# Optimization experiments

Measured on AMD Instinct MI355X. Metric: run time of the kernel, lower is better.

The kernel has to match this reference:

```python
import jax, jax.numpy as jnp
import numpy as np
import math
from jax import lax

D = 256      # d_model = out_channel
NH = 8       # n_heads
DEP = D // NH
DFF = 1024
B = 48       # conv batch == attended axis in this model
CIN = 32
HW = 32
S = 30 * 30  # (HW-2)**2 after 3x3 valid conv
OUT = 1
FMAX = float(np.finfo(np.float32).max)


def _p(k, shp, scale=0.02):
    return jax.random.normal(k, shp, jnp.float32) * scale


def setup_inputs():
    key = jax.random.key(0)
    ks = jax.random.split(key, 34)
    return {
        'X_en': jax.random.normal(ks[0], (B, CIN, HW, HW), jnp.float32),
        'X_de': jax.random.normal(ks[1], (B, CIN, HW, HW), jnp.float32),
        'conv1_w': _p(ks[2], (D, CIN, 3, 3)), 'conv1_b': _p(ks[3], (D,)),
        'conv2_w': _p(ks[4], (D, D, 3, 3)), 'conv2_b': _p(ks[5], (D,)),
        'enc_wq': _p(ks[6], (D, D)), 'enc_wk': _p(ks[7], (D, D)), 'enc_wv': _p(ks[8], (D, D)),
        'enc_rel_w': _p(ks[9], (S, NH, DEP, B)),
        'enc_ffn_w1': _p(ks[10], (DFF, D)), 'enc_ffn_b1': _p(ks[11], (DFF,)),
        'enc_ffn_w2': _p(ks[12], (D, DFF)), 'enc_ffn_b2': _p(ks[13], (D,)),
        'dec_m_wq': _p(ks[14], (D, D)), 'dec_m_wk': _p(ks[15], (D, D)), 'dec_m_wv': _p(ks[16], (D, D)),
        'dec_m_rel_w': _p(ks[17], (S, NH, DEP, B)),
        'dec_m_lin1_w': _p(ks[18], (B, B)), 'dec_m_lin1_b': _p(ks[19], (B,)),
        'dec_m_lin2_w': _p(ks[20], (B, B)), 'dec_m_lin2_b': _p(ks[21], (B,)),
        'dec_c_wq': _p(ks[22], (D, D)), 'dec_c_wk': _p(ks[23], (D, D)), 'dec_c_wv': _p(ks[24], (D, D)),
        'dec_c_rel_w': _p(ks[25], (S, NH, DEP, B)),
        'dec_ffn_w1': _p(ks[26], (DFF, D)), 'dec_ffn_b1': _p(ks[27], (DFF,)),
        'dec_ffn_w2': _p(ks[28], (D, DFF)), 'dec_ffn_b2': _p(ks[29], (D,)),
        'out_w': _p(ks[30], (OUT, D)), 'out_b': _p(ks[31], (OUT,)),
    }


def _ln(x, eps=1e-5):
    m = jnp.mean(x, -1, keepdims=True)
    v = jnp.mean((x - m) ** 2, -1, keepdims=True)
    return (x - m) / jnp.sqrt(v + eps)


def _skew(q, w):
    # Music-Transformer relative-position skew: matmul + pad + reshape + slice
    emd = jnp.einsum('shbd,shdj->shbj', q, w)  # (S,NH,b,b)
    s, h, i, j = emd.shape
    l = i + j - 1
    x = jnp.concatenate([emd, jnp.zeros_like(emd)], -1).reshape(s, h, -1)
    pad = (-x.shape[-1]) % l
    x = jnp.pad(x, ((0, 0), (0, 0), (0, pad)))
    return x.reshape(s, h, -1, l)[:, :, :i, i - 1:]


def _mha(xq, xk, xv, wq, wk, wv, rel_w, lins=None):
    b, sl, d = xq.shape
    # raw view (not transpose): (b,sl,d) -> (sl,b,NH,DEP), then swap to (sl,NH,b,DEP)
    q = (xq @ wq.T).reshape(sl, b, NH, DEP).swapaxes(1, 2)
    k = (xk @ wk.T).reshape(sl, b, NH, DEP).swapaxes(1, 2)
    v = (xv @ wv.T).reshape(sl, b, NH, DEP).swapaxes(1, 2)
    scores = jnp.einsum('shid,shjd->shij', q, k) / math.sqrt(DEP)  # (sl,NH,b,b)
    if lins is not None:  # masked path: per-call linears + causal mask
        l1w, l1b, l2w, l2b = lins
        qk = scores @ l1w.T + l1b
        qk = jnp.swapaxes(qk, 2, 3) @ l2w.T + l2b
        mask = jnp.triu(jnp.full((b, b), -FMAX, jnp.float32), 1)
        bmm = qk + mask
    else:
        bmm = scores  # linear1/linear2 outputs are discarded when mask=False
    attn = jax.nn.softmax(bmm + _skew(q, rel_w), axis=0)  # softmax over dim 0 (S)
    out = jnp.einsum('shij,shjd->shid', attn, v)  # (sl,NH,b,DEP)
    return out.reshape(b, sl, NH * DEP)  # view(a_s[2], a_s[0], -1)


def reference(X_en, X_de, conv1_w, conv1_b, conv2_w, conv2_b, enc_wq, enc_wk, enc_wv, enc_rel_w, enc_ffn_w1, enc_ffn_b1, enc_ffn_w2, enc_ffn_b2, dec_m_wq, dec_m_wk, dec_m_wv, dec_m_rel_w, dec_m_lin1_w, dec_m_lin1_b, dec_m_lin2_w, dec_m_lin2_b, dec_c_wq, dec_c_wk, dec_c_wv, dec_c_rel_w, dec_ffn_w1, dec_ffn_b1, dec_ffn_w2, dec_ffn_b2, out_w, out_b):
    def conv(x, w, b_, pad):
        y = lax.conv_general_dilated(x, w, (1, 1), [(pad, pad), (pad, pad)],
                                     dimension_numbers=('NCHW', 'OIHW', 'NCHW'))
        return y + b_[None, :, None, None]

    def convs(x):
        return conv(conv(x, conv1_w, conv1_b, 0), conv2_w, conv2_b, 1)

    xpe = convs(X_en)
    xpd = convs(X_de)
    b, d, h, w = xpe.shape
    x_en = xpe.reshape(b, h * w, d)  # raw reshape as in torch source
    x_de = xpd.reshape(b, h * w, d)
    # encoder layer
    a = _mha(x_en, x_en, x_en, enc_wq, enc_wk, enc_wv, enc_rel_w)
    o1 = _ln(x_en + a)
    f = jax.nn.relu(o1 @ enc_ffn_w1.T + enc_ffn_b1) @ enc_ffn_w2.T + enc_ffn_b2
    enc_out = _ln(o1 + f)
    # decoder layer
    m = _mha(x_de, x_de, x_de, dec_m_wq, dec_m_wk, dec_m_wv, dec_m_rel_w,
             (dec_m_lin1_w, dec_m_lin1_b, dec_m_lin2_w, dec_m_lin2_b))
    h1 = _ln(x_de + m)
    c = _mha(h1, enc_out, enc_out, dec_c_wq, dec_c_wk, dec_c_wv, dec_c_rel_w)
    h2 = _ln(c + h1)
    f2 = jax.nn.relu(h2 @ dec_ffn_w1.T + dec_ffn_b1) @ dec_ffn_w2.T + dec_ffn_b2
    h3 = _ln(h2 + f2)
    y = h3 @ out_w.T + out_b
    return jax.nn.softmax(y, axis=0)
```

## Files before the change

### kernel.cpp

```cpp
#include <hip/hip_runtime.h>
#include <float.h>

typedef __bf16 bf16;
typedef __attribute__((ext_vector_type(8))) __bf16 bf16x8;
typedef __attribute__((ext_vector_type(4))) __bf16 bf16x4;
typedef __attribute__((ext_vector_type(4))) float f32x4;

__device__ __forceinline__ int imin(int a, int b) { return a < b ? a : b; }

__device__ __forceinline__ void gl2lds(const bf16* g, bf16* l) {
  __builtin_amdgcn_global_load_lds(
      (const __attribute__((address_space(1))) void*)g,
      (__attribute__((address_space(3))) void*)l, 16, 0, 0);
}

__global__ void k_prep_misc(bf16* zp, const float* __restrict__ l1w,
                            const float* __restrict__ l2w,
                            bf16* __restrict__ L1p, bf16* __restrict__ L2p) {
  zp[threadIdx.x] = (bf16)0.0f;
  for (int i = threadIdx.x; i < 3456; i += 256) {
    int r = i / 72, c = i - r * 72;
    L1p[i] = (c < 48) ? (bf16)l1w[r * 48 + c] : (bf16)0.0f;
    L2p[i] = (c < 48) ? (bf16)l2w[r * 48 + c] : (bf16)0.0f;
  }
}

struct CastSegs { const float* s[13]; bf16* d[13]; int n[13]; };
__global__ void k_cast_all(CastSegs sg, int total) {
  int i = blockIdx.x * 256 + threadIdx.x;
  if (i >= total) return;
  for (int k = 0; k < 13; ++k) {
    if (i < sg.n[k]) { sg.d[k][i] = (bf16)sg.s[k][i]; return; }
    i -= sg.n[k];
  }
}

__global__ __launch_bounds__(256) void k_prep_rel(const float* __restrict__ rel,
                                                  bf16* __restrict__ RelT) {
  __shared__ float tile[32 * 49];
  const int t = threadIdx.x;
  for (int u = 0; u < 8; ++u) {
    const size_t sh = (size_t)blockIdx.x * 8 + u;
    const float* src = rel + sh * 1536;
    bf16* dst = RelT + sh * 1536;
    __syncthreads();
    for (int i = t; i < 1536; i += 256) {
      int k = i / 48, j = i - k * 48;
      tile[k * 49 + j] = src[i];
    }
    __syncthreads();
    for (int i = t; i < 1536; i += 256) {
      int j = i >> 5, k = i & 31;
      dst[i] = (bf16)tile[k * 49 + j];
    }
  }
}

__global__ void k_prep_x(const float* __restrict__ XE, const float* __restrict__ XD,
                         bf16* __restrict__ XR) {
  int idx = blockIdx.x * 256 + threadIdx.x;
  if (idx >= 96 * 1024 * 32) return;
  int b = idx >> 15, r = idx & 32767, pos = r >> 5, ic = r & 31;
  const float* X = (b < 48) ? XE : XD;
  int bl = (b < 48) ? b : b - 48;
  XR[idx] = (bf16)X[((size_t)(bl * 32 + ic) << 10) + pos];
}

__global__ void k_pack_conv(const float* __restrict__ w, bf16* __restrict__ dst,
                            int OC, int IC, int total) {
  int idx = blockIdx.x * 256 + threadIdx.x;
  if (idx >= total) return;
  int t = idx / (OC * IC);
  int rem = idx - t * OC * IC;
  int oc = rem / IC, ic = rem - oc * IC;
  dst[idx] = (bf16)w[(size_t)(oc * IC + ic) * 9 + t];
}

__global__ __launch_bounds__(256, 2) void k_gemm128(
    const bf16* __restrict__ A, const bf16* __restrict__ A2,
    const bf16* __restrict__ B, const bf16* __restrict__ B2, int nsplit,
    const float* __restrict__ bias, bf16* __restrict__ C,
    int M, int N, int K, int relu, int ldc, int coff) {
  __shared__ alignas(16) bf16 SM[32768];
  const int t = threadIdx.x, wave = t >> 6;
  const int lane = t & 63, fr = lane & 15, kq = lane >> 4;
  const int wm = wave & 1, wn = wave >> 1;
  const int m0 = blockIdx.x * 128, n0 = blockIdx.y * 128;
  const bf16* Ause = A; const bf16* Buse = B; int nloc = n0;
  if (n0 >= nsplit) { Ause = A2; Buse = B2; nloc = n0 - nsplit; }
  const int srow = t >> 3;
  const int sg8 = (((t & 7) ^ (srow & 7)) << 3);
  const bf16* gA[4]; const bf16* gB[4];
#pragma unroll
  for (int r = 0; r < 4; ++r) {
    gA[r] = Ause + (size_t)imin(m0 + r * 32 + srow, M - 1) * K + sg8;
    gB[r] = Buse + (size_t)(nloc + r * 32 + srow) * K + sg8;
  }
  const int swz = (kq ^ (fr & 7)) << 3;
  const int aoff = (wm * 64 + fr) * 64 + swz;
  const int boff = 8192 + (wn * 64 + fr) * 64 + swz;
  f32x4 acc[4][4] = {};
  const int NU = K >> 6;
  {
    bf16* db = SM + wave * 512;
#pragma unroll
    for (int r = 0; r < 4; ++r) gl2lds(gA[r], db + r * 2048);
#pragma unroll
    for (int r = 0; r < 4; ++r) gl2lds(gB[r], db + 8192 + r * 2048);
  }
  __syncthreads();
  for (int u = 0; u < NU; ++u) {
    const int cur = u & 1;
    if (u + 1 < NU) {
      bf16* db = SM + (cur ^ 1) * 16384 + wave * 512;
      const int kb = (u + 1) << 6;
#pragma unroll
      for (int r = 0; r < 4; ++r) gl2lds(gA[r] + kb, db + r * 2048);
#pragma unroll
      for (int r = 0; r < 4; ++r) gl2lds(gB[r] + kb, db + 8192 + r * 2048);
    }
    const bf16* buf = SM + cur * 16384;
    bf16x8 af[2][4], bw[2][4];
#pragma unroll
    for (int kk = 0; kk < 2; ++kk) {
      const int xo = kk << 5;
#pragma unroll
      for (int mt = 0; mt < 4; ++mt)
        af[kk][mt] = *(const bf16x8*)(buf + ((aoff + mt * 1024) ^ xo));
#pragma unroll
      for (int nt = 0; nt < 4; ++nt)
        bw[kk][nt] = *(const bf16x8*)(buf + ((boff + nt * 1024) ^ xo));
    }
#pragma unroll
    for (int kk = 0; kk < 2; ++kk)
#pragma unroll
      for (int mt = 0; mt < 4; ++mt)
#pragma unroll
        for (int nt = 0; nt < 4; ++nt)
          acc[mt][nt] = __builtin_amdgcn_mfma_f32_16x16x32_bf16(af[kk][mt], bw[kk][nt], acc[mt][nt], 0, 0, 0);
    __syncthreads();
  }
  bf16* Cst = SM;
  for (int half = 0; half < 2; ++half) {
    if (wm == half) {
      for (int mt = 0; mt < 4; ++mt)
        for (int nt = 0; nt < 4; ++nt) {
          int n = n0 + wn * 64 + nt * 16 + fr;
          float bv = bias ? bias[n] : 0.0f;
          for (int r = 0; r < 4; ++r) {
            float v = acc[mt][nt][r] + bv;
            if (relu) v = fmaxf(v, 0.0f);
            Cst[(mt * 16 + kq * 4 + r) * 128 + wn * 64 + nt * 16 + fr] = (bf16)v;
          }
        }
    }
    __syncthreads();
    for (int i = t; i < 1024; i += 256) {
      int r = i >> 4, cs = i & 15;
      int gm = m0 + half * 64 + r;
      if (gm < M)
        *(bf16x8*)(C + (size_t)gm * ldc + coff + n0 + cs * 8) = *(const bf16x8*)(Cst + r * 128 + cs * 8);
    }
    __syncthreads();
  }
}

template <int CIN, int PAD, int SRCW, int SRCROWS, int CHECK, int TRANS, int MTOT>
__global__ __launch_bounds__(256, 2) void k_conv128(
    const bf16* __restrict__ A, const bf16* __restrict__ Bp,
    const float* __restrict__ bias, bf16* __restrict__ C,
    const bf16* __restrict__ zpage) {
  __shared__ alignas(16) bf16 SM[8192];
  bf16* As = SM;
  bf16* Bs = SM + 4096;
  const int t = threadIdx.x, wave = t >> 6;
  const int lane = t & 63, fr = lane & 15, kq = lane >> 4;
  const int wm = wave & 1, wn = wave >> 1;
  const int m0 = blockIdx.x * 128, n0 = blockIdx.y * 128;
  const int srow = t >> 2, kseg = (t & 3) * 8;
  f32x4 acc[4][4] = {};
  int bb[2], yy[2], xx[2];
  for (int hf = 0; hf < 2; ++hf) {
    int m = imin(m0 + hf * 64 + srow, MTOT - 1);
    int b = m / 900, p = m - b * 900;
    bb[hf] = b; yy[hf] = p / 30; xx[hf] = p - (p / 30) * 30;
  }
  bf16* sA0 = As + wave * 512;
  bf16* sA1 = As + 2048 + wave * 512;
  bf16* sB0 = Bs + wave * 512;
  bf16* sB1 = Bs + 2048 + wave * 512;
  for (int k0 = 0; k0 < CIN; k0 += 32) {
    for (int t9 = 0; t9 < 9; ++t9) {
      const int ky = t9 / 3, kx = t9 - ky * 3;
      const bf16* ga[2];
      for (int hf = 0; hf < 2; ++hf) {
        int sy = yy[hf] + ky - PAD, sx = xx[hf] + kx - PAD;
        bool valid = !CHECK || (sy >= 0 && sy < SRCW && sx >= 0 && sx < SRCW);
        ga[hf] = (valid ? A + (size_t)(bb[hf] * SRCROWS + sy * SRCW + sx) * CIN : zpage) + kseg;
      }
      const bf16* gb = Bp + (size_t)(t9 * 256 + n0 + srow) * CIN + kseg;
      gl2lds(ga[0] + k0, sA0);
      gl2lds(ga[1] + k0, sA1);
      gl2lds(gb + k0, sB0);
      gl2lds(gb + (size_t)64 * CIN + k0, sB1);
      __syncthreads();
      bf16x8 af[4], bw[4];
      for (int mt = 0; mt < 4; ++mt)
        af[mt] = *(const bf16x8*)(As + (wm * 64 + mt * 16 + fr) * 32 + kq * 8);
      for (int nt = 0; nt < 4; ++nt)
        bw[nt] = *(const bf16x8*)(Bs + (wn * 64 + nt * 16 + fr) * 32 + kq * 8);
      for (int mt = 0; mt < 4; ++mt)
        for (int nt = 0; nt < 4; ++nt)
          acc[mt][nt] = __builtin_amdgcn_mfma_f32_16x16x32_bf16(af[mt], bw[nt], acc[mt][nt], 0, 0, 0);
      __syncthreads();
    }
  }
  bf16* Cst = SM;
  for (int half = 0; half < 2; ++half) {
    if (wm == half) {
      for (int mt = 0; mt < 4; ++mt)
        for (int nt = 0; nt < 4; ++nt) {
          int n = n0 + wn * 64 + nt * 16 + fr;
          float bv = bias[n];
          for (int r = 0; r < 4; ++r) {
            float v = acc[mt][nt][r] + bv;
            if (TRANS)
              Cst[(wn * 64 + nt * 16 + fr) * 64 + mt * 16 + kq * 4 + r] = (bf16)v;
            else
              Cst[(mt * 16 + kq * 4 + r) * 128 + wn * 64 + nt * 16 + fr] = (bf16)v;
          }
        }
    }
    __syncthreads();
    if (TRANS) {
      for (int i = t; i < 2048; i += 256) {
        int oc = i >> 4, pc = i & 15;
        int gm = m0 + half * 64 + pc * 4;
        if (gm < MTOT) {
          int b = gm / 900, p = gm - b * 900;
          *(bf16x4*)(C + (size_t)(b * 256 + n0 + oc) * 900 + p) = *(const bf16x4*)(Cst + oc * 64 + pc * 4);
        }
      }
    } else {
      for (int i = t; i < 1024; i += 256) {
        int r = i >> 4, cs = i & 15;
        int gm = m0 + half * 64 + r;
        if (gm < MTOT)
          *(bf16x8*)(C + (size_t)gm * 256 + n0 + cs * 8) = *(const bf16x8*)(Cst + r * 128 + cs * 8);
      }
    }
    __syncthreads();
  }
}

__global__ __launch_bounds__(256, 2) void k_conv2x(
    const bf16* __restrict__ A, const bf16* __restrict__ Bp,
    const float* __restrict__ bias, bf16* __restrict__ C,
    const bf16* __restrict__ zpage) {
  __shared__ alignas(16) bf16 SM[32768];
  const int t = threadIdx.x, wave = t >> 6;
  const int lane = t & 63, fr = lane & 15, kq = lane >> 4;
  const int wm = wave & 1, wn = wave >> 1;
  const int m0 = blockIdx.x * 128, n0 = blockIdx.y * 128;
  const int srow = t >> 3;
  const int sg8 = (((t & 7) ^ (srow & 7)) << 3);
  int pb[4], py[4], px[4];
#pragma unroll
  for (int r = 0; r < 4; ++r) {
    int m = imin(m0 + r * 32 + srow, 86399);
    int b = m / 900, p = m - b * 900;
    pb[r] = b * 900; py[r] = p / 30; px[r] = p - (p / 30) * 30;
  }
  const int swz = (kq ^ (fr & 7)) << 3;
  const int aoff = (wm * 64 + fr) * 64 + swz;
  const int boff = 8192 + (wn * 64 + fr) * 64 + swz;
  f32x4 acc[4][4] = {};
  auto stage = [&](int u, int bsel) {
    const int t9 = u >> 2, k0c = (u & 3) << 6;
    const int ky = t9 / 3, kx = t9 - ky * 3;
    bf16* db = SM + bsel * 16384 + wave * 512;
#pragma unroll
    for (int r = 0; r < 4; ++r) {
      int sy = py[r] + ky - 1, sx = px[r] + kx - 1;
      bool valid = (sy >= 0 && sy < 30 && sx >= 0 && sx < 30);
      const bf16* g = valid ? (A + (size_t)(pb[r] + sy * 30 + sx) * 256 + k0c + sg8)
                            : (zpage + sg8);
      gl2lds(g, db + r * 2048);
    }
    const bf16* gb = Bp + (size_t)(t9 * 256 + n0 + srow) * 256 + k0c + sg8;
#pragma unroll
    for (int r = 0; r < 4; ++r)
      gl2lds(gb + (size_t)r * 32 * 256, db + 8192 + r * 2048);
  };
  stage(0, 0);
  __syncthreads();
  for (int u = 0; u < 36; ++u) {
    const int cur = u & 1;
    if (u < 35) stage(u + 1, cur ^ 1);
    const bf16* buf = SM + cur * 16384;
    bf16x8 af[2][4], bw[2][4];
#pragma unroll
    for (int kk = 0; kk < 2; ++kk) {
      const int xo = kk << 5;
#pragma unroll
      for (int mt = 0; mt < 4; ++mt)
        af[kk][mt] = *(const bf16x8*)(buf + ((aoff + mt * 1024) ^ xo));
#pragma unroll
      for (int nt = 0; nt < 4; ++nt)
        bw[kk][nt] = *(const bf16x8*)(buf + ((boff + nt * 1024) ^ xo));
    }
#pragma unroll
    for (int kk = 0; kk < 2; ++kk)
#pragma unroll
      for (int mt = 0; mt < 4; ++mt)
#pragma unroll
        for (int nt = 0; nt < 4; ++nt)
          acc[mt][nt] = __builtin_amdgcn_mfma_f32_16x16x32_bf16(af[kk][mt], bw[kk][nt], acc[mt][nt], 0, 0, 0);
    __syncthreads();
  }
  bf16* Cst = SM;
  for (int half = 0; half < 2; ++half) {
    if (wm == half) {
      for (int mt = 0; mt < 4; ++mt)
        for (int nt = 0; nt < 4; ++nt) {
          int n = n0 + wn * 64 + nt * 16 + fr;
          float bv = bias[n];
          for (int r = 0; r < 4; ++r) {
            float v = acc[mt][nt][r] + bv;
            Cst[(wn * 64 + nt * 16 + fr) * 64 + mt * 16 + kq * 4 + r] = (bf16)v;
          }
        }
    }
    __syncthreads();
    for (int i = t; i < 2048; i += 256) {
      int oc = i >> 4, pc = i & 15;
      int gm = m0 + half * 64 + pc * 4;
      int b = gm / 900, p = gm - b * 900;
      *(bf16x4*)(C + (size_t)(b * 256 + n0 + oc) * 900 + p) = *(const bf16x4*)(Cst + oc * 64 + pc * 4);
    }
    __syncthreads();
  }
}

template <int MASKED>
__global__ __launch_bounds__(256, MASKED ? 4 : 5) void k_attn_z(
    const bf16* __restrict__ QKV, const bf16* __restrict__ RelT, bf16* __restrict__ Z,
    const bf16* __restrict__ L1p, const bf16* __restrict__ L2p,
    const float* __restrict__ l1b, const float* __restrict__ l2b) {
  __shared__ alignas(16) bf16 QKs[2][48 * 40];
  __shared__ float EMD[48 * 49];
  __shared__ alignas(16) bf16 zst[48 * 48];
  __shared__ alignas(16) bf16 Sc[MASKED ? 48 * 72 : 8];
  __shared__ alignas(16) bf16 T2b[MASKED ? 48 * 72 : 8];
  const int sh = blockIdx.x, s = sh >> 3, h = sh & 7;
  const int t = threadIdx.x, wave = t >> 6, lane = t & 63, fr = lane & 15, kq = lane >> 4;
  const float scale = 0.17677669529663687f;
  for (int c = t; c < 384; c += 256) {
    int half = c >= 192 ? 1 : 0, cc = c - half * 192;
    int row = cc >> 2, seg = cc & 3;
    *(bf16x8*)(&QKs[half][row * 40 + seg * 8]) =
        *(const bf16x8*)(QKV + (size_t)(s * 48 + row) * 768 + half * 256 + h * 32 + seg * 8);
  }
  if constexpr (MASKED) {
    for (int i = t; i < 768; i += 256) {
      int r = i >> 4, c = 48 + (i & 15);
      Sc[r * 72 + c] = (bf16)0.0f;
      T2b[r * 72 + c] = (bf16)0.0f;
    }
  }
  __syncthreads();
  const bf16* relb = RelT + (size_t)sh * 1536;
  f32x4 sreg[3];
  int u = 0;
  for (int t9 = wave; t9 < 9; t9 += 4, ++u) {
    int ti = t9 / 3, tj = t9 - ti * 3;
    bf16x8 af = *(const bf16x8*)(&QKs[0][(ti * 16 + fr) * 40 + kq * 8]);
    bf16x8 bk = *(const bf16x8*)(&QKs[1][(tj * 16 + fr) * 40 + kq * 8]);
    bf16x8 rf = *(const bf16x8*)(relb + (tj * 16 + fr) * 32 + kq * 8);
    f32x4 sacc = {}, eacc = {};
    sacc = __builtin_amdgcn_mfma_f32_16x16x32_bf16(af, bk, sacc, 0, 0, 0);
    eacc = __builtin_amdgcn_mfma_f32_16x16x32_bf16(af, rf, eacc, 0, 0, 0);
    for (int r = 0; r < 4; ++r)
      EMD[(ti * 16 + kq * 4 + r) * 49 + tj * 16 + fr] = eacc[r];
    if constexpr (MASKED) {
      for (int r = 0; r < 4; ++r)
        Sc[(ti * 16 + kq * 4 + r) * 72 + tj * 16 + fr] = (bf16)(sacc[r] * scale);
    } else {
      for (int r = 0; r < 4; ++r) sreg[u][r] = sacc[r] * scale;
    }
  }
  __syncthreads();
  if constexpr (!MASKED) {
    u = 0;
    for (int t9 = wave; t9 < 9; t9 += 4, ++u) {
      int ti = t9 / 3, tj = t9 - ti * 3;
      for (int r = 0; r < 4; ++r) {
        int i = ti * 16 + kq * 4 + r, j = tj * 16 + fr;
        float v = sreg[u][r];
        if (j <= i) v += EMD[i * 49 + 47 + j - i];
        zst[i * 48 + j] = (bf16)v;
      }
    }
  } else {
    for (int t9 = wave; t9 < 9; t9 += 4) {
      int ti = t9 / 3, tj = t9 - ti * 3;
      f32x4 a2 = {};
      for (int k0 = 0; k0 < 64; k0 += 32) {
        bf16x8 af = *(const bf16x8*)(Sc + (ti * 16 + fr) * 72 + k0 + kq * 8);
        bf16x8 bw = *(const bf16x8*)(L1p + (tj * 16 + fr) * 72 + k0 + kq * 8);
        a2 = __builtin_amdgcn_mfma_f32_16x16x32_bf16(af, bw, a2, 0, 0, 0);
      }
      for (int r = 0; r < 4; ++r) {
        int i = ti * 16 + kq * 4 + r, a = tj * 16 + fr;
        T2b[a * 72 + i] = (bf16)(a2[r] + l1b[a]);
      }
    }
    __syncthreads();
    for (int t9 = wave; t9 < 9; t9 += 4) {
      int ti = t9 / 3, tj = t9 - ti * 3;
      f32x4 a2 = {};
      for (int k0 = 0; k0 < 64; k0 += 32) {
        bf16x8 af = *(const bf16x8*)(T2b + (ti * 16 + fr) * 72 + k0 + kq * 8);
        bf16x8 bw = *(const bf16x8*)(L2p + (tj * 16 + fr) * 72 + k0 + kq * 8);
        a2 = __builtin_amdgcn_mfma_f32_16x16x32_bf16(af, bw, a2, 0, 0, 0);
      }
      for (int r = 0; r < 4; ++r) {
        int aa = ti * 16 + kq * 4 + r, cc = tj * 16 + fr;
        float v;
        if (cc > aa) v = -10000.0f;
        else v = a2[r] + l2b[cc] + EMD[aa * 49 + 47 + cc - aa];
        zst[aa * 48 + cc] = (bf16)v;
      }
    }
  }
  __syncthreads();
  bf16* zb = Z + (size_t)sh * 2304;
  for (int c = t; c < 288; c += 256)
    *(bf16x8*)(zb + c * 8) = *(const bf16x8*)(zst + c * 8);
}

__global__ __launch_bounds__(256) void k_colstats(const bf16* __restrict__ Z,
                                                  float* __restrict__ Mc, float* __restrict__ Ic) {
  __shared__ float rm[32][72], rs[32][72];
  const int t = threadIdx.x, cg = t & 7, sg = t >> 3;
  const bf16* p = Z + blockIdx.x * 64 + cg * 8;
  const int s0 = sg * 29, s1 = imin(900, s0 + 29);
  float m[8], ss[8];
  for (int e = 0; e < 8; ++e) { m[e] = -FLT_MAX; ss[e] = 0.0f; }
  for (int s = s0; s < s1; ++s) {
    bf16x8 zv = *(const bf16x8*)(p + (size_t)s * 18432);
    for (int e = 0; e < 8; ++e) {
      float v = (float)zv[e];
      if (v > m[e]) { ss[e] *= __expf(m[e] - v); m[e] = v; }
      ss[e] += __expf(v - m[e]);
    }
  }
  for (int e = 0; e < 8; ++e) { rm[sg][cg * 8 + e] = m[e]; rs[sg][cg * 8 + e] = ss[e]; }
  __syncthreads();
  if (t < 64) {
    float M2 = -FLT_MAX;
    for (int g = 0; g < 32; ++g) M2 = fmaxf(M2, rm[g][t]);
    float S2 = 0.0f;
    for (int g = 0; g < 32; ++g) S2 += rs[g][t] * __expf(rm[g][t] - M2);
    Mc[blockIdx.x * 64 + t] = M2;
    Ic[blockIdx.x * 64 + t] = 1.0f / S2;
  }
}

__global__ __launch_bounds__(256, 6) void k_attn_av(
    const bf16* __restrict__ Z, const bf16* __restrict__ QKV,
    const float* __restrict__ Mc, const float* __restrict__ Ic, bf16* __restrict__ O) {
  __shared__ alignas(16) bf16 Ps[48 * 72];
  __shared__ alignas(16) bf16 Vt[32 * 72];
  __shared__ alignas(16) bf16 Ost[48 * 32];
  const int sh = blockIdx.x, s = sh >> 3, h = sh & 7;
  const int t = threadIdx.x, wave = t >> 6, lane = t & 63, fr = lane & 15, kq = lane >> 4;
  for (int i = t; i < 768; i += 256) Ps[(i >> 4) * 72 + 48 + (i & 15)] = (bf16)0.0f;
  for (int i = t; i < 512; i += 256) Vt[(i >> 4) * 72 + 48 + (i & 15)] = (bf16)0.0f;
  const bf16* zb = Z + (size_t)sh * 2304;
  const float* mc = Mc + h * 2304;
  const float* ic = Ic + h * 2304;
  for (int c = t; c < 288; c += 256) {
    int r = c / 6, seg = c - r * 6;
    int idx = r * 48 + seg * 8;
    bf16x8 zv = *(const bf16x8*)(zb + idx);
    f32x4 m0v = *(const f32x4*)(mc + idx), m1v = *(const f32x4*)(mc + idx + 4);
    f32x4 i0v = *(const f32x4*)(ic + idx), i1v = *(const f32x4*)(ic + idx + 4);
    bf16x8 pv;
    for (int e = 0; e < 4; ++e) pv[e] = (bf16)(__expf((float)zv[e] - m0v[e]) * i0v[e]);
    for (int e = 0; e < 4; ++e) pv[4 + e] = (bf16)(__expf((float)zv[4 + e] - m1v[e]) * i1v[e]);
    *(bf16x8*)(Ps + r * 72 + seg * 8) = pv;
  }
  for (int c = t; c < 192; c += 256) {
    int j = c >> 2, seg = c & 3;
    bf16x8 v = *(const bf16x8*)(QKV + (size_t)(s * 48 + j) * 768 + 512 + h * 32 + seg * 8);
    for (int e = 0; e < 8; ++e) Vt[(seg * 8 + e) * 72 + j] = v[e];
  }
  __syncthreads();
  for (int t6 = wave; t6 < 6; t6 += 4) {
    int ti = t6 >> 1, td = t6 & 1;
    f32x4 a2 = {};
    for (int k0 = 0; k0 < 64; k0 += 32) {
      bf16x8 af = *(const bf16x8*)(Ps + (ti * 16 + fr) * 72 + k0 + kq * 8);
      bf16x8 bv = *(const bf16x8*)(Vt + (td * 16 + fr) * 72 + k0 + kq * 8);
      a2 = __builtin_amdgcn_mfma_f32_16x16x32_bf16(af, bv, a2, 0, 0, 0);
    }
    for (int r = 0; r < 4; ++r)
      Ost[(ti * 16 + kq * 4 + r) * 32 + td * 16 + fr] = (bf16)a2[r];
  }
  __syncthreads();
  bf16* ob = O + (size_t)sh * 1536;
  for (int c = t; c < 192; c += 256)
    *(bf16x8*)(ob + c * 8) = *(const bf16x8*)(Ost + c * 8);
}

__global__ __launch_bounds__(256) void k_add_ln(
    const bf16* __restrict__ Xa, const bf16* __restrict__ Xb, bf16* __restrict__ out) {
  const int t = threadIdx.x, lane = t & 63, w = t >> 6;
  const size_t off = ((size_t)blockIdx.x * 4 + w) * 256 + lane * 4;
  bf16x4 av = *(const bf16x4*)(Xa + off);
  bf16x4 bv = *(const bf16x4*)(Xb + off);
  f32x4 x;
  for (int c = 0; c < 4; ++c) x[c] = (float)av[c] + (float)bv[c];
  float sum = x[0] + x[1] + x[2] + x[3];
  for (int o = 1; o < 64; o <<= 1) sum += __shfl_xor(sum, o);
  float mean = sum * (1.0f / 256.0f);
  float q = 0.0f;
  for (int c = 0; c < 4; ++c) { float d = x[c] - mean; q += d * d; }
  for (int o = 1; o < 64; o <<= 1) q += __shfl_xor(q, o);
  float rstd = rsqrtf(q * (1.0f / 256.0f) + 1e-5f);
  bf16x4 y;
  for (int c = 0; c < 4; ++c) y[c] = (bf16)((x[c] - mean) * rstd);
  *(bf16x4*)(out + off) = y;
}

__global__ __launch_bounds__(256) void k_ydot(
    const bf16* __restrict__ H, const float* __restrict__ w,
    const float* __restrict__ b, float* __restrict__ Y) {
  const int t = threadIdx.x, lane = t & 63, wv = t >> 6;
  const size_t row = (size_t)blockIdx.x * 4 + wv;
  bf16x4 hx = *(const bf16x4*)(H + row * 256 + lane * 4);
  f32x4 ww = *(const f32x4*)(w + lane * 4);
  float s = (float)hx[0] * ww[0] + (float)hx[1] * ww[1] + (float)hx[2] * ww[2] + (float)hx[3] * ww[3];
  for (int o = 1; o < 64; o <<= 1) s += __shfl_xor(s, o);
  if (lane == 0) Y[row] = s + b[0];
}

__global__ void k_softmax48(const float* __restrict__ Y, float* __restrict__ O) {
  int ss = blockIdx.x * 256 + threadIdx.x;
  if (ss >= 900) return;
  float m = -FLT_MAX;
  for (int b = 0; b < 48; ++b) m = fmaxf(m, Y[b * 900 + ss]);
  float sum = 0.0f;
  for (int b = 0; b < 48; ++b) sum += __expf(Y[b * 900 + ss] - m);
  float inv = 1.0f / sum;
  for (int b = 0; b < 48; ++b) O[b * 900 + ss] = __expf(Y[b * 900 + ss] - m) * inv;
}

extern "C" void kernel_launch(void* const* d_in, const int* in_sizes, int n_in,
                              void* d_out, int out_size, void* d_ws, size_t ws_size,
                              hipStream_t stream) {
  (void)in_sizes; (void)n_in; (void)out_size;
  const float* X_en = (const float*)d_in[0];
  const float* X_de = (const float*)d_in[1];
  const float* conv1_w = (const float*)d_in[2];
  const float* conv1_b = (const float*)d_in[3];
  const float* conv2_w = (const float*)d_in[4];
  const float* conv2_b = (const float*)d_in[5];
  const float* enc_wq = (const float*)d_in[6];
  const float* enc_wk = (const float*)d_in[7];
  const float* enc_wv = (const float*)d_in[8];
  const float* enc_rel = (const float*)d_in[9];
  const float* enc_f1w = (const float*)d_in[10];
  const float* enc_f1b = (const float*)d_in[11];
  const float* enc_f2w = (const float*)d_in[12];
  const float* enc_f2b = (const float*)d_in[13];
  const float* dm_wq = (const float*)d_in[14];
  const float* dm_wk = (const float*)d_in[15];
  const float* dm_wv = (const float*)d_in[16];
  const float* dm_rel = (const float*)d_in[17];
  const float* dm_l1w = (const float*)d_in[18];
  const float* dm_l1b = (const float*)d_in[19];
  const float* dm_l2w = (const float*)d_in[20];
  const float* dm_l2b = (const float*)d_in[21];
  const float* dc_wq = (const float*)d_in[22];
  const float* dc_wk = (const float*)d_in[23];
  const float* dc_wv = (const float*)d_in[24];
  const float* dc_rel = (const float*)d_in[25];
  const float* d_f1w = (const float*)d_in[26];
  const float* d_f1b = (const float*)d_in[27];
  const float* d_f2w = (const float*)d_in[28];
  const float* d_f2b = (const float*)d_in[29];
  const float* out_w = (const float*)d_in[30];
  const float* out_b = (const float*)d_in[31];
  float* OUT = (float*)d_out;

  const size_t SLOT = 22118400;
  char* ws = (char*)d_ws;
  size_t o = 0;
  bf16* S1 = (bf16*)(ws + o); o += SLOT;
  bf16* S2 = (bf16*)(ws + o); o += SLOT;
  bf16* S3 = (bf16*)(ws + o); o += SLOT;
  bf16* S4 = (bf16*)(ws + o); o += SLOT;
  bf16* S5 = (bf16*)(ws + o); o += SLOT;
  char* U = ws + o; o += 33177600 + 3 * SLOT;
  bf16* Zb = (bf16*)U;
  bf16* QKV = (bf16*)(U + 33177600);
  bf16* XR = (bf16*)U;
  bf16* C1R = (bf16*)(U + 12582912);
  bf16* HID = (bf16*)U;
  bf16* wa = (bf16*)(ws + o); o += 4603904 + 16384;
  float* Y = (float*)(ws + o); o += 172800;
  if (ws_size < o) return;

  bf16* zpage = (bf16*)Y;
  float* encM = (float*)S4; float* encI = encM + 18432;
  float* dmM  = (float*)S3; float* dmI  = dmM + 18432;
  float* crM  = (float*)S2; float* crI  = crM + 18432;
  bf16* encRel = S3;
  bf16* dmRel  = S5;
  bf16* crRel  = S3;

  bf16* c1p = wa;
  bf16* c2p = wa + 73728;
  bf16* EQKVw = wa + 663552;
  bf16* MQKVw = wa + 860160;
  bf16* cqw = wa + 1056768;
  bf16* CKVw = wa + 1122304;
  bf16* ef1 = wa + 1253376;
  bf16* ef2 = wa + 1515520;
  bf16* df1 = wa + 1777664;
  bf16* df2 = wa + 2039808;
  bf16* L1p = wa + 2301952;
  bf16* L2p = wa + 2305408;

  auto gemm = [&](const bf16* A, const bf16* B, const float* bias, bf16* C,
                  int M, int N, int K, int relu, int ldc, int coff) {
    k_gemm128<<<dim3((M + 127) / 128, N / 128), dim3(256), 0, stream>>>(
        A, A, B, B, N, bias, C, M, N, K, relu, ldc, coff);
  };

  k_prep_misc<<<dim3(1), dim3(256), 0, stream>>>(zpage, dm_l1w, dm_l2w, L1p, L2p);
  k_pack_conv<<<dim3(288), dim3(256), 0, stream>>>(conv1_w, c1p, 256, 32, 73728);
  k_pack_conv<<<dim3(2304), dim3(256), 0, stream>>>(conv2_w, c2p, 256, 256, 589824);
  {
    CastSegs sg;
    const float* srcs[13] = {enc_wq, enc_wk, enc_wv, dm_wq, dm_wk, dm_wv, dc_wq,
                             dc_wk, dc_wv, enc_f1w, enc_f2w, d_f1w, d_f2w};
    bf16* dsts[13] = {EQKVw, EQKVw + 65536, EQKVw + 131072, MQKVw, MQKVw + 65536,
                      MQKVw + 131072, cqw, CKVw, CKVw + 65536, ef1, ef2, df1, df2};
    int ns[13] = {65536, 65536, 65536, 65536, 65536, 65536, 65536, 65536, 65536,
                  262144, 262144, 262144, 262144};
    int total = 0;
    for (int k = 0; k < 13; ++k) { sg.s[k] = srcs[k]; sg.d[k] = dsts[k]; sg.n[k] = ns[k]; total += ns[k]; }
    k_cast_all<<<dim3((total + 255) / 256), dim3(256), 0, stream>>>(sg, total);
  }

  k_prep_x<<<dim3(12288), dim3(256), 0, stream>>>(X_en, X_de, XR);
  k_conv128<32, 0, 32, 1024, 0, 0, 86400><<<dim3(675, 2), dim3(256), 0, stream>>>(
      XR, c1p, conv1_b, C1R, zpage);
  k_conv2x<<<dim3(675, 2), dim3(256), 0, stream>>>(C1R, c2p, conv2_b, S1, zpage);

  gemm(S1, EQKVw, nullptr, QKV, 43200, 768, 256, 0, 768, 0);
  k_prep_rel<<<dim3(900), dim3(256), 0, stream>>>(enc_rel, encRel);
  k_attn_z<0><<<dim3(7200), dim3(256), 0, stream>>>(QKV, encRel, Zb, nullptr, nullptr, nullptr, nullptr);
  k_colstats<<<dim3(288), dim3(256), 0, stream>>>(Zb, encM, encI);
  k_attn_av<<<dim3(7200), dim3(256), 0, stream>>>(Zb, QKV, encM, encI, S5);
  k_add_ln<<<dim3(10800), dim3(256), 0, stream>>>(S1, S5, S3);
  gemm(S3, ef1, enc_f1b, HID, 43200, 1024, 256, 1, 1024, 0);
  gemm(HID, ef2, enc_f2b, S5, 43200, 256, 1024, 0, 256, 0);
  k_add_ln<<<dim3(10800), dim3(256), 0, stream>>>(S3, S5, S1);

  gemm(S2, MQKVw, nullptr, QKV, 43200, 768, 256, 0, 768, 0);
  k_prep_rel<<<dim3(900), dim3(256), 0, stream>>>(dm_rel, dmRel);
  k_attn_z<1><<<dim3(7200), dim3(256), 0, stream>>>(QKV, dmRel, Zb, L1p, L2p, dm_l1b, dm_l2b);
  k_colstats<<<dim3(288), dim3(256), 0, stream>>>(Zb, dmM, dmI);
  k_attn_av<<<dim3(7200), dim3(256), 0, stream>>>(Zb, QKV, dmM, dmI, S5);
  k_add_ln<<<dim3(10800), dim3(256), 0, stream>>>(S2, S5, S4);

  k_gemm128<<<dim3(338, 6), dim3(256), 0, stream>>>(
      S4, S1, cqw, CKVw, 256, nullptr, QKV, 43200, 768, 256, 0, 768, 0);
  k_prep_rel<<<dim3(900), dim3(256), 0, stream>>>(dc_rel, crRel);
  k_attn_z<0><<<dim3(7200), dim3(256), 0, stream>>>(QKV, crRel, Zb, nullptr, nullptr, nullptr, nullptr);
  k_colstats<<<dim3(288), dim3(256), 0, stream>>>(Zb, crM, crI);
  k_attn_av<<<dim3(7200), dim3(256), 0, stream>>>(Zb, QKV, crM, crI, S5);
  k_add_ln<<<dim3(10800), dim3(256), 0, stream>>>(S5, S4, S3);

  gemm(S3, df1, d_f1b, HID, 43200, 1024, 256, 1, 1024, 0);
  gemm(HID, df2, d_f2b, S5, 43200, 256, 1024, 0, 256, 0);
  k_add_ln<<<dim3(10800), dim3(256), 0, stream>>>(S3, S5, S4);
  k_ydot<<<dim3(10800), dim3(256), 0, stream>>>(S4, out_w, out_b, Y);
  k_softmax48<<<dim3(4), dim3(256), 0, stream>>>(Y, OUT);
}
```

Baseline: 1.106 ms.

## Single-buffer LDS in GEMM and conv2 kernels, pad epilogue staging

Drops double-buffered LDS prefetching in k_gemm128 and k_conv2x in favour of a single 32KB buffer with load-sync-compute-sync per K step. It also reorders the conv K loop so channel blocks are outermost, and pads the epilogue staging rows (136/68) to reduce LDS bank conflicts. Halving LDS and shrinking fragment register arrays aims at higher occupancy, but global-load latency is no longer overlapped with MFMA work inside a block. The staging buffer still fits, since 64 rows x 136 = 8704 and 128 x 68 = 8704 elements are under 16384.

```diff
diff --git a/kernel.cpp b/kernel.cpp
--- a/kernel.cpp
+++ b/kernel.cpp
@@ -81,7 +81,7 @@
     const bf16* __restrict__ B, const bf16* __restrict__ B2, int nsplit,
     const float* __restrict__ bias, bf16* __restrict__ C,
     int M, int N, int K, int relu, int ldc, int coff) {
-  __shared__ alignas(16) bf16 SM[32768];
+  __shared__ alignas(16) bf16 SM[16384];
   const int t = threadIdx.x, wave = t >> 6;
   const int lane = t & 63, fr = lane & 15, kq = lane >> 4;
   const int wm = wave & 1, wn = wave >> 1;
@@ -100,44 +100,29 @@
   const int aoff = (wm * 64 + fr) * 64 + swz;
   const int boff = 8192 + (wn * 64 + fr) * 64 + swz;
   f32x4 acc[4][4] = {};
-  const int NU = K >> 6;
-  {
+  for (int k0 = 0; k0 < K; k0 += 64) {
     bf16* db = SM + wave * 512;
 #pragma unroll
-    for (int r = 0; r < 4; ++r) gl2lds(gA[r], db + r * 2048);
-#pragma unroll
-    for (int r = 0; r < 4; ++r) gl2lds(gB[r], db + 8192 + r * 2048);
-  }
-  __syncthreads();
-  for (int u = 0; u < NU; ++u) {
-    const int cur = u & 1;
-    if (u + 1 < NU) {
-      bf16* db = SM + (cur ^ 1) * 16384 + wave * 512;
-      const int kb = (u + 1) << 6;
-#pragma unroll
-      for (int r = 0; r < 4; ++r) gl2lds(gA[r] + kb, db + r * 2048);
-#pragma unroll
-      for (int r = 0; r < 4; ++r) gl2lds(gB[r] + kb, db + 8192 + r * 2048);
-    }
-    const bf16* buf = SM + cur * 16384;
-    bf16x8 af[2][4], bw[2][4];
+    for (int r = 0; r < 4; ++r) gl2lds(gA[r] + k0, db + r * 2048);
+#pragma unroll
+    for (int r = 0; r < 4; ++r) gl2lds(gB[r] + k0, db + 8192 + r * 2048);
+    __syncthreads();
 #pragma unroll
     for (int kk = 0; kk < 2; ++kk) {
       const int xo = kk << 5;
+      bf16x8 af[4], bw[4];
 #pragma unroll
       for (int mt = 0; mt < 4; ++mt)
-        af[kk][mt] = *(const bf16x8*)(buf + ((aoff + mt * 1024) ^ xo));
+        af[mt] = *(const bf16x8*)(SM + ((aoff + mt * 1024) ^ xo));
 #pragma unroll
       for (int nt = 0; nt < 4; ++nt)
-        bw[kk][nt] = *(const bf16x8*)(buf + ((boff + nt * 1024) ^ xo));
-    }
-#pragma unroll
-    for (int kk = 0; kk < 2; ++kk)
+        bw[nt] = *(const bf16x8*)(SM + ((boff + nt * 1024) ^ xo));
 #pragma unroll
       for (int mt = 0; mt < 4; ++mt)
 #pragma unroll
         for (int nt = 0; nt < 4; ++nt)
-          acc[mt][nt] = __builtin_amdgcn_mfma_f32_16x16x32_bf16(af[kk][mt], bw[kk][nt], acc[mt][nt], 0, 0, 0);
+          acc[mt][nt] = __builtin_amdgcn_mfma_f32_16x16x32_bf16(af[mt], bw[nt], acc[mt][nt], 0, 0, 0);
+    }
     __syncthreads();
   }
   bf16* Cst = SM;
@@ -150,7 +135,7 @@
           for (int r = 0; r < 4; ++r) {
             float v = acc[mt][nt][r] + bv;
             if (relu) v = fmaxf(v, 0.0f);
-            Cst[(mt * 16 + kq * 4 + r) * 128 + wn * 64 + nt * 16 + fr] = (bf16)v;
+            Cst[(mt * 16 + kq * 4 + r) * 136 + wn * 64 + nt * 16 + fr] = (bf16)v;
           }
         }
     }
@@ -159,7 +144,7 @@
       int r = i >> 4, cs = i & 15;
       int gm = m0 + half * 64 + r;
       if (gm < M)
-        *(bf16x8*)(C + (size_t)gm * ldc + coff + n0 + cs * 8) = *(const bf16x8*)(Cst + r * 128 + cs * 8);
+        *(bf16x8*)(C + (size_t)gm * ldc + coff + n0 + cs * 8) = *(const bf16x8*)(Cst + r * 136 + cs * 8);
     }
     __syncthreads();
   }
@@ -257,7 +242,7 @@
     const bf16* __restrict__ A, const bf16* __restrict__ Bp,
     const float* __restrict__ bias, bf16* __restrict__ C,
     const bf16* __restrict__ zpage) {
-  __shared__ alignas(16) bf16 SM[32768];
+  __shared__ alignas(16) bf16 SM[16384];
   const int t = threadIdx.x, wave = t >> 6;
   const int lane = t & 63, fr = lane & 15, kq = lane >> 4;
   const int wm = wave & 1, wn = wave >> 1;
@@ -275,48 +260,41 @@
   const int aoff = (wm * 64 + fr) * 64 + swz;
   const int boff = 8192 + (wn * 64 + fr) * 64 + swz;
   f32x4 acc[4][4] = {};
-  auto stage = [&](int u, int bsel) {
-    const int t9 = u >> 2, k0c = (u & 3) << 6;
-    const int ky = t9 / 3, kx = t9 - ky * 3;
-    bf16* db = SM + bsel * 16384 + wave * 512;
-#pragma unroll
-    for (int r = 0; r < 4; ++r) {
-      int sy = py[r] + ky - 1, sx = px[r] + kx - 1;
-      bool valid = (sy >= 0 && sy < 30 && sx >= 0 && sx < 30);
-      const bf16* g = valid ? (A + (size_t)(pb[r] + sy * 30 + sx) * 256 + k0c + sg8)
-                            : (zpage + sg8);
-      gl2lds(g, db + r * 2048);
-    }
-    const bf16* gb = Bp + (size_t)(t9 * 256 + n0 + srow) * 256 + k0c + sg8;
-#pragma unroll
-    for (int r = 0; r < 4; ++r)
-      gl2lds(gb + (size_t)r * 32 * 256, db + 8192 + r * 2048);
-  };
-  stage(0, 0);
-  __syncthreads();
-  for (int u = 0; u < 36; ++u) {
-    const int cur = u & 1;
-    if (u < 35) stage(u + 1, cur ^ 1);
-    const bf16* buf = SM + cur * 16384;
-    bf16x8 af[2][4], bw[2][4];
-#pragma unroll
-    for (int kk = 0; kk < 2; ++kk) {
-      const int xo = kk << 5;
-#pragma unroll
-      for (int mt = 0; mt < 4; ++mt)
-        af[kk][mt] = *(const bf16x8*)(buf + ((aoff + mt * 1024) ^ xo));
-#pragma unroll
-      for (int nt = 0; nt < 4; ++nt)
-        bw[kk][nt] = *(const bf16x8*)(buf + ((boff + nt * 1024) ^ xo));
-    }
-#pragma unroll
-    for (int kk = 0; kk < 2; ++kk)
-#pragma unroll
-      for (int mt = 0; mt < 4; ++mt)
+  for (int k0 = 0; k0 < 256; k0 += 64) {
+    for (int t9 = 0; t9 < 9; ++t9) {
+      const int ky = t9 / 3, kx = t9 - ky * 3;
+      bf16* db = SM + wave * 512;
+#pragma unroll
+      for (int r = 0; r < 4; ++r) {
+        int sy = py[r] + ky - 1, sx = px[r] + kx - 1;
+        bool valid = (sy >= 0 && sy < 30 && sx >= 0 && sx < 30);
+        const bf16* g = valid ? (A + (size_t)(pb[r] + sy * 30 + sx) * 256 + k0 + sg8)
+                              : (zpage + sg8);
+        gl2lds(g, db + r * 2048);
+      }
+#pragma unroll
+      for (int r = 0; r < 4; ++r)
+        gl2lds(Bp + (size_t)(t9 * 256 + n0 + r * 32 + srow) * 256 + k0 + sg8,
+               db + 8192 + r * 2048);
+      __syncthreads();
+#pragma unroll
+      for (int kk = 0; kk < 2; ++kk) {
+        const int xo = kk << 5;
+        bf16x8 af[4], bw[4];
+#pragma unroll
+        for (int mt = 0; mt < 4; ++mt)
+          af[mt] = *(const bf16x8*)(SM + ((aoff + mt * 1024) ^ xo));
 #pragma unroll
         for (int nt = 0; nt < 4; ++nt)
-          acc[mt][nt] = __builtin_amdgcn_mfma_f32_16x16x32_bf16(af[kk][mt], bw[kk][nt], acc[mt][nt], 0, 0, 0);
-    __syncthreads();
+          bw[nt] = *(const bf16x8*)(SM + ((boff + nt * 1024) ^ xo));
+#pragma unroll
+        for (int mt = 0; mt < 4; ++mt)
+#pragma unroll
+          for (int nt = 0; nt < 4; ++nt)
+            acc[mt][nt] = __builtin_amdgcn_mfma_f32_16x16x32_bf16(af[mt], bw[nt], acc[mt][nt], 0, 0, 0);
+      }
+      __syncthreads();
+    }
   }
   bf16* Cst = SM;
   for (int half = 0; half < 2; ++half) {
@@ -327,7 +305,7 @@
           float bv = bias[n];
           for (int r = 0; r < 4; ++r) {
             float v = acc[mt][nt][r] + bv;
-            Cst[(wn * 64 + nt * 16 + fr) * 64 + mt * 16 + kq * 4 + r] = (bf16)v;
+            Cst[(wn * 64 + nt * 16 + fr) * 68 + mt * 16 + kq * 4 + r] = (bf16)v;
           }
         }
     }
@@ -336,7 +314,7 @@
       int oc = i >> 4, pc = i & 15;
       int gm = m0 + half * 64 + pc * 4;
       int b = gm / 900, p = gm - b * 900;
-      *(bf16x4*)(C + (size_t)(b * 256 + n0 + oc) * 900 + p) = *(const bf16x4*)(Cst + oc * 64 + pc * 4);
+      *(bf16x4*)(C + (size_t)(b * 256 + n0 + oc) * 900 + p) = *(const bf16x4*)(Cst + oc * 68 + pc * 4);
     }
     __syncthreads();
   }
```

Result: faster. 1.007 ms (median of 2 runs) (-8.9%).
